# Kernel optimization log

Measured on AMD Instinct MI355X. Metric: run time of the kernel, lower is better.

Reference implementation:

```python
import jax, jax.numpy as jnp
import numpy as np

B, T_ENC, D_IN, H, C, STEPS = 512, 64, 512, 512, 38, 26


def setup_inputs() -> dict:
    key = jax.random.key(0)
    ks = jax.random.split(key, 12)
    s = 0.05
    return {
        "encoder_output": jax.random.normal(ks[0], (B, T_ENC, D_IN), jnp.float32),
        "text": jax.random.randint(ks[1], (B, STEPS), 0, C),
        "w_i2h": jax.random.normal(ks[2], (H, D_IN), jnp.float32) * s,
        "w_h2h": jax.random.normal(ks[3], (H, H), jnp.float32) * s,
        "b_h2h": jax.random.normal(ks[4], (H,), jnp.float32) * s,
        "w_score": jax.random.normal(ks[5], (1, H), jnp.float32) * s,
        "w_ih": jax.random.normal(ks[6], (4 * H, D_IN + C), jnp.float32) * s,
        "w_hh": jax.random.normal(ks[7], (4 * H, H), jnp.float32) * s,
        "b_ih": jax.random.normal(ks[8], (4 * H,), jnp.float32) * s,
        "b_hh": jax.random.normal(ks[9], (4 * H,), jnp.float32) * s,
        "w_gen": jax.random.normal(ks[10], (C, H), jnp.float32) * s,
        "b_gen": jax.random.normal(ks[11], (C,), jnp.float32) * s,
    }


def reference(encoder_output, text, w_i2h, w_h2h, b_h2h, w_score, w_ih, w_hh,
              b_ih, b_hh, w_gen, b_gen):
    # i2h(batch_H) is step-invariant -> hoist out of the decode loop (same math).
    H_proj = jnp.einsum('btd,hd->bth', encoder_output, w_i2h)  # [B,T,H]
    onehots = jax.nn.one_hot(text, C, dtype=encoder_output.dtype)  # [B,S,C]
    oh_seq = jnp.swapaxes(onehots, 0, 1)  # [S,B,C]

    def step(carry, oh):
        h, c = carry
        hp = (h @ w_h2h.T + b_h2h)[:, None, :]                 # [B,1,H]
        e = jnp.tanh(H_proj + hp) @ w_score[0]                  # [B,T]
        alpha = jax.nn.softmax(e, axis=1)                       # [B,T]
        context = jnp.einsum('bt,btd->bd', alpha, encoder_output)
        x = jnp.concatenate([context, oh], axis=1)              # [B,D+C]
        gates = x @ w_ih.T + b_ih + h @ w_hh.T + b_hh           # [B,4H]
        i_g, f_g, g_g, o_g = jnp.split(gates, 4, axis=1)
        c_new = jax.nn.sigmoid(f_g) * c + jax.nn.sigmoid(i_g) * jnp.tanh(g_g)
        h_new = jax.nn.sigmoid(o_g) * jnp.tanh(c_new)
        return (h_new, c_new), h_new

    z = jnp.zeros((encoder_output.shape[0], w_h2h.shape[0]), encoder_output.dtype)
    _, hs = jax.lax.scan(step, (z, z), oh_seq)                  # hs: [S,B,H]
    hiddens = jnp.swapaxes(hs, 0, 1)                            # [B,S,H]
    probs = hiddens @ w_gen.T + b_gen                           # [B,S,C]
    return probs
```

## Files before the change

### kernel.cpp

```cpp
#include <hip/hip_runtime.h>

typedef __attribute__((ext_vector_type(8))) short bf16x8;
typedef __attribute__((ext_vector_type(4))) float f32x4;
typedef __attribute__((ext_vector_type(4))) int   i32x4;

#define DEV static __device__ __forceinline__

constexpr int BATCH = 512;
constexpr int TENC  = 64;
constexpr int DIN   = 512;
constexpr int HDIM  = 512;
constexpr int NCLS  = 38;
constexpr int STEPS = 26;
constexpr int NG    = 4 * HDIM;

constexpr size_t HP_OFF   = 0;
constexpr size_t HP_SZ    = (size_t)BATCH * TENC * HDIM * 2;
constexpr size_t ENC_OFF  = HP_OFF + HP_SZ;
constexpr size_t ENC_SZ   = (size_t)BATCH * TENC * DIN * 2;
constexpr size_t A2_OFF   = ENC_OFF + ENC_SZ;
constexpr size_t A2_SZ    = (size_t)2 * BATCH * 1024 * 2;
constexpr size_t HP32_OFF = A2_OFF + A2_SZ;
constexpr size_t HP32_SZ  = (size_t)BATCH * HDIM * 4;
constexpr size_t B2R_OFF  = HP32_OFF + HP32_SZ;
constexpr size_t B2R_SZ   = (size_t)NG * 1024 * 2;
constexpr size_t WI2H_OFF = B2R_OFF + B2R_SZ;
constexpr size_t WI2H_SZ  = (size_t)HDIM * DIN * 2;
constexpr size_t B3_OFF   = WI2H_OFF + WI2H_SZ;
constexpr size_t B3_SZ    = (size_t)576 * HDIM * 2;
constexpr size_t WOH_OFF  = B3_OFF + B3_SZ;
constexpr size_t WOH_SZ   = (size_t)NG * NCLS * 4;
constexpr size_t BIAS_OFF = WOH_OFF + WOH_SZ;
constexpr size_t BIAS_SZ  = (size_t)NG * 4;
constexpr size_t HSEQ_OFF = BIAS_OFF + BIAS_SZ;
constexpr size_t HSEQ_SZ  = (size_t)STEPS * BATCH * HDIM * 2;
constexpr size_t BAR_OFF  = HSEQ_OFF + HSEQ_SZ;
constexpr size_t BAR_SZ   = 32768;

DEV float bf2f(unsigned short s) {
    unsigned u = ((unsigned)s) << 16;
    return __builtin_bit_cast(float, u);
}
DEV unsigned short f2bf(float f) {
    unsigned u = __builtin_bit_cast(unsigned, f);
    u = (u + 0x7fffu + ((u >> 16) & 1u)) >> 16;
    return (unsigned short)u;
}
DEV float sigmoid_f(float x) { return 1.f / (1.f + __expf(-x)); }
DEV float tanh_f(float x) {
    x = fminf(fmaxf(x, -15.f), 15.f);
    float e = __expf(2.f * x);
    return (e - 1.f) / (e + 1.f);
}

DEV unsigned aload(const unsigned* p) {
    return __hip_atomic_load(p, __ATOMIC_RELAXED, __HIP_MEMORY_SCOPE_AGENT);
}
DEV unsigned long long aload64(const unsigned long long* p) {
    return __hip_atomic_load(p, __ATOMIC_RELAXED, __HIP_MEMORY_SCOPE_AGENT);
}
DEV float aloadf(const float* p) {
    return __hip_atomic_load(p, __ATOMIC_RELAXED, __HIP_MEMORY_SCOPE_AGENT);
}
DEV void astore(unsigned* p, unsigned v) {
    __hip_atomic_store(p, v, __ATOMIC_RELAXED, __HIP_MEMORY_SCOPE_AGENT);
}
DEV void astoref(float* p, float v) {
    __hip_atomic_store(p, v, __ATOMIC_RELAXED, __HIP_MEMORY_SCOPE_AGENT);
}
DEV bf16x8 mk_frag(unsigned long long lo, unsigned long long hi) {
    union { unsigned long long q[2]; bf16x8 v; } u;
    u.q[0] = lo; u.q[1] = hi;
    return u.v;
}

DEV void gbar(unsigned* gb, int j, unsigned g) {
    __syncthreads();
    if (threadIdx.x == 0) {
        const int sg = j & 3;
        unsigned* sub  = gb + sg * 32;
        unsigned* root = gb + 128;
        unsigned* genp = gb + 160 + sg * 32;
        bool flipped = false;
        if (__hip_atomic_fetch_add(sub, 1u, __ATOMIC_RELAXED, __HIP_MEMORY_SCOPE_AGENT) == g * 8u - 1u) {
            if (__hip_atomic_fetch_add(root, 1u, __ATOMIC_RELAXED, __HIP_MEMORY_SCOPE_AGENT) == g * 4u - 1u) {
                #pragma unroll
                for (int i = 0; i < 4; i++) astore(gb + 160 + i * 32, g);
                flipped = true;
            }
        }
        if (!flipped) {
            while (aload(genp) < g) __builtin_amdgcn_s_sleep(1);
        }
    }
    __syncthreads();
}

__global__ void conv_bf16_kernel(const float* __restrict__ in,
                                 unsigned short* __restrict__ out, int n4) {
    int i = blockIdx.x * blockDim.x + threadIdx.x;
    int stride = gridDim.x * blockDim.x;
    for (; i < n4; i += stride) {
        float4 v = ((const float4*)in)[i];
        ushort4 o;
        o.x = f2bf(v.x); o.y = f2bf(v.y); o.z = f2bf(v.z); o.w = f2bf(v.w);
        ((ushort4*)out)[i] = o;
    }
}

__global__ void build_b2r_kernel(const float* __restrict__ w_ih, const float* __restrict__ w_hh,
                                 const float* __restrict__ b_ih, const float* __restrict__ b_hh,
                                 unsigned short* __restrict__ B2r, float* __restrict__ woh,
                                 float* __restrict__ bias2r) {
    int np = blockIdx.x;
    int u = np >> 2, g = np & 3;
    int src = g * 512 + u;
    for (int k = threadIdx.x; k < 512; k += blockDim.x) {
        B2r[np * 1024 + k]       = f2bf(w_ih[src * 550 + k]);
        B2r[np * 1024 + 512 + k] = f2bf(w_hh[src * 512 + k]);
    }
    if (threadIdx.x < NCLS) woh[np * NCLS + threadIdx.x] = w_ih[src * 550 + 512 + threadIdx.x];
    if (threadIdx.x == 0)   bias2r[np] = b_ih[src] + b_hh[src];
}

__global__ void build_b3_kernel(const float* __restrict__ w_h2h, const float* __restrict__ w_gen,
                                unsigned short* __restrict__ B3) {
    int n = blockIdx.x;
    for (int k = threadIdx.x; k < 512; k += blockDim.x) {
        float v = 0.f;
        if (n < 512)      v = w_h2h[n * 512 + k];
        else if (n < 550) v = w_gen[(n - 512) * 512 + k];
        B3[n * 512 + k] = f2bf(v);
    }
}

__global__ void init_state_kernel(unsigned short* __restrict__ A2,
                                  unsigned* __restrict__ bar) {
    int b = blockIdx.x;
    for (int j = threadIdx.x; j < 512; j += blockDim.x)
        A2[b * 1024 + 512 + j] = 0;
    if (b == 0)
        for (int j = threadIdx.x; j < 8192; j += blockDim.x) bar[j] = 0;
}

template<int BM, int BN, int WN, int FRM, int FRN>
DEV void gemm_core(const unsigned short* __restrict__ A, int ldA,
                   const unsigned short* __restrict__ Bm, int ldB, int K,
                   int m0, int n0, unsigned short* __restrict__ lA,
                   unsigned short* __restrict__ lB, f32x4 acc[FRM][FRN]) {
    constexpr int LSTR = 40;
    const int tid  = threadIdx.x;
    const int lane = tid & 63;
    const int wid  = tid >> 6;
    const int wm = wid / WN, wn = wid % WN;
    const int fr_row = lane & 15;
    const int fr_kb  = (lane >> 4) * 8;

    for (int k0 = 0; k0 < K; k0 += 32) {
        for (int u = tid; u < BM * 4; u += 256) {
            int r = u >> 2, cb = u & 3;
            *(i32x4*)(lA + r * LSTR + cb * 8) =
                *(const i32x4*)(A + (size_t)(m0 + r) * ldA + k0 + cb * 8);
        }
        for (int u = tid; u < BN * 4; u += 256) {
            int r = u >> 2, cb = u & 3;
            *(i32x4*)(lB + r * LSTR + cb * 8) =
                *(const i32x4*)(Bm + (size_t)(n0 + r) * ldB + k0 + cb * 8);
        }
        __syncthreads();
        bf16x8 af[FRM], bfv[FRN];
        #pragma unroll
        for (int i = 0; i < FRM; i++)
            af[i] = *(const bf16x8*)(lA + (wm * FRM * 16 + i * 16 + fr_row) * LSTR + fr_kb);
        #pragma unroll
        for (int j = 0; j < FRN; j++)
            bfv[j] = *(const bf16x8*)(lB + (wn * FRN * 16 + j * 16 + fr_row) * LSTR + fr_kb);
        #pragma unroll
        for (int i = 0; i < FRM; i++)
            #pragma unroll
            for (int j = 0; j < FRN; j++)
                acc[i][j] = __builtin_amdgcn_mfma_f32_16x16x32_bf16(af[i], bfv[j], acc[i][j], 0, 0, 0);
        __syncthreads();
    }
}

__global__ __launch_bounds__(256) void gemm_bf16out_kernel(
    const unsigned short* __restrict__ A, int ldA,
    const unsigned short* __restrict__ Bm, int ldB,
    unsigned short* __restrict__ C, int ldC, int K) {
    constexpr int BM = 128, BN = 128, FRM = 4, FRN = 4;
    __shared__ __align__(16) unsigned short lA[BM * 40], lB[BN * 40];
    int m0 = blockIdx.x * BM, n0 = blockIdx.y * BN;
    f32x4 acc[FRM][FRN] = {};
    gemm_core<BM, BN, 2, FRM, FRN>(A, ldA, Bm, ldB, K, m0, n0, lA, lB, acc);
    const int lane = threadIdx.x & 63, wid = threadIdx.x >> 6;
    const int wm = wid >> 1, wn = wid & 1;
    #pragma unroll
    for (int i = 0; i < FRM; i++)
        #pragma unroll
        for (int j = 0; j < FRN; j++)
            #pragma unroll
            for (int r = 0; r < 4; r++) {
                int m = m0 + wm * FRM * 16 + i * 16 + (lane >> 4) * 4 + r;
                int n = n0 + wn * FRN * 16 + j * 16 + (lane & 15);
                C[(size_t)m * ldC + n] = f2bf(acc[i][j][r]);
            }
}

__global__ __launch_bounds__(256) void probs_kernel(
    const unsigned short* __restrict__ hseq,
    const unsigned short* __restrict__ Bg,
    const float* __restrict__ b_gen, float* __restrict__ out) {
    __shared__ __align__(16) unsigned short lA[64 * 40], lB[64 * 40];
    int m0 = blockIdx.x * 64;
    f32x4 acc[2][2] = {};
    gemm_core<64, 64, 2, 2, 2>(hseq, 512, Bg, 512, 512, m0, 0, lA, lB, acc);
    const int lane = threadIdx.x & 63, wid = threadIdx.x >> 6;
    const int wm = wid >> 1, wn = wid & 1;
    #pragma unroll
    for (int i = 0; i < 2; i++)
        #pragma unroll
        for (int j = 0; j < 2; j++)
            #pragma unroll
            for (int r = 0; r < 4; r++) {
                int m = m0 + wm * 32 + i * 16 + (lane >> 4) * 4 + r;
                int n = wn * 32 + j * 16 + (lane & 15);
                if (n < NCLS) {
                    int ss = m >> 9, b = m & 511;
                    out[((size_t)b * STEPS + ss) * NCLS + n] = acc[i][j][r] + b_gen[n];
                }
            }
}

__global__ __launch_bounds__(512, 2) void decode_kernel(
    const unsigned short* __restrict__ Hp,
    const unsigned short* __restrict__ enc,
    unsigned short* __restrict__ A2,
    float* __restrict__ hpb,
    const unsigned short* __restrict__ B2r,
    const float* __restrict__ bias2r,
    const float* __restrict__ woh,
    const unsigned short* __restrict__ B3,
    const float* __restrict__ b_h2h,
    const float* __restrict__ w_score,
    const int* __restrict__ text,
    unsigned short* __restrict__ hseq,
    unsigned* __restrict__ bar) {
    __shared__ __align__(16) unsigned short lB2w[64 * 1032];
    __shared__ __align__(16) char scr[17408];

    const int bid  = blockIdx.x;
    const int tid  = threadIdx.x;
    const int lane = tid & 63, wid = tid >> 6;
    const int grp = bid >> 5;
    const int j   = bid & 31;
    const int gm0 = grp * 64;
    const int ng0 = j * 64;
    const int ncol0 = j * 16;
    const int mi = wid & 3;
    const int kh = wid >> 2;
    unsigned* gb = bar + grp * 1024;

    for (int u = tid; u < 8192; u += 512) {
        int r = u >> 7, cb = u & 127;
        *(i32x4*)(lB2w + r * 1032 + cb * 8) =
            *(const i32x4*)(B2r + (size_t)(ng0 + r) * 1024 + cb * 8);
    }

    float c0 = 0.f, c1 = 0.f;
    unsigned gen = 0;

    float* pbuf  = (float*)scr;
    float* e_lds = (float*)scr;
    float* al_lds = e_lds + 128;
    float* gbuf  = (float*)scr;

    for (int s = 0; s < STEPS; ++s) {
        unsigned short* A2cur = A2 + (size_t)(s & 1) * BATCH * 1024;
        unsigned short* A2nxt = A2 + (size_t)((s + 1) & 1) * BATCH * 1024;

        {
            const int arow = gm0 + mi * 16 + (lane & 15);
            const unsigned long long* Ah = (const unsigned long long*)
                (A2cur + (size_t)arow * 1024 + 512 + kh * 256 + (lane >> 4) * 8);
            const unsigned short* wrow = B3 + (size_t)(ncol0 + (lane & 15)) * 512
                                            + kh * 256 + (lane >> 4) * 8;
            unsigned long long h0v[8], h1v[8];
            #pragma unroll
            for (int kc = 0; kc < 8; ++kc) {
                h0v[kc] = aload64(Ah + kc * 8);
                h1v[kc] = aload64(Ah + kc * 8 + 1);
            }
            f32x4 acc = {};
            #pragma unroll
            for (int kc = 0; kc < 8; ++kc) {
                bf16x8 af = mk_frag(h0v[kc], h1v[kc]);
                bf16x8 bf = *(const bf16x8*)(wrow + kc * 32);
                acc = __builtin_amdgcn_mfma_f32_16x16x32_bf16(af, bf, acc, 0, 0, 0);
            }
            if (kh == 1) {
                #pragma unroll
                for (int r = 0; r < 4; r++)
                    pbuf[mi * 272 + ((lane >> 4) * 4 + r) * 17 + (lane & 15)] = acc[r];
            }
            __syncthreads();
            if (kh == 0) {
                #pragma unroll
                for (int r = 0; r < 4; r++) {
                    int row = (lane >> 4) * 4 + r, col = lane & 15;
                    float v = acc[r] + pbuf[mi * 272 + row * 17 + col] + b_h2h[ncol0 + col];
                    astoref(hpb + (size_t)(gm0 + mi * 16 + row) * 512 + ncol0 + col, v);
                }
            }
        }
        gbar(gb, j, ++gen);

        f32x4 gacc[4] = {};
        {
            unsigned long long g0v[16], g1v[16];
            if (kh == 1) {
                const unsigned long long* Ag = (const unsigned long long*)
                    (A2cur + (size_t)(gm0 + mi * 16 + (lane & 15)) * 1024 + 512 + (lane >> 4) * 8);
                #pragma unroll
                for (int kc = 0; kc < 16; ++kc) {
                    g0v[kc] = aload64(Ag + kc * 8);
                    g1v[kc] = aload64(Ag + kc * 8 + 1);
                }
            }

            const int half = tid >> 8, t4 = tid & 255, w4 = t4 >> 6;
            const int b = gm0 + 2 * j + half;
            float hp8[8], ws8[8];
            #pragma unroll
            for (int q = 0; q < 8; q++) hp8[q] = aloadf(hpb + (size_t)b * 512 + lane * 8 + q);
            {
                const float4* wsp = (const float4*)(w_score + lane * 8);
                float4 w0 = wsp[0], w1 = wsp[1];
                ws8[0] = w0.x; ws8[1] = w0.y; ws8[2] = w0.z; ws8[3] = w0.w;
                ws8[4] = w1.x; ws8[5] = w1.y; ws8[6] = w1.z; ws8[7] = w1.w;
            }
            for (int t = w4; t < 64; t += 4) {
                bf16x8 hv = *(const bf16x8*)(Hp + ((size_t)b * 64 + t) * 512 + lane * 8);
                float a = 0.f;
                #pragma unroll
                for (int q = 0; q < 8; q++)
                    a += ws8[q] * tanh_f(hp8[q] + bf2f((unsigned short)hv[q]));
                #pragma unroll
                for (int off = 32; off > 0; off >>= 1) a += __shfl_down(a, off);
                if (lane == 0) e_lds[half * 64 + t] = a;
            }
            __syncthreads();
            if (w4 == 0) {
                float v = e_lds[half * 64 + lane];
                float m = v;
                #pragma unroll
                for (int off = 32; off > 0; off >>= 1) m = fmaxf(m, __shfl_xor(m, off));
                float ex = __expf(v - m);
                float sum = ex;
                #pragma unroll
                for (int off = 32; off > 0; off >>= 1) sum += __shfl_xor(sum, off);
                al_lds[half * 64 + lane] = ex / sum;
            }
            __syncthreads();
            float a0 = 0.f, a1 = 0.f;
            const unsigned short* erow = enc + (size_t)b * 64 * 512 + t4 * 2;
            #pragma unroll 8
            for (int t = 0; t < 64; t++) {
                float al = al_lds[half * 64 + t];
                unsigned pv = *(const unsigned*)(erow + (size_t)t * 512);
                a0 += al * bf2f((unsigned short)(pv & 0xffffu));
                a1 += al * bf2f((unsigned short)(pv >> 16));
            }
            unsigned pk = ((unsigned)f2bf(a1) << 16) | (unsigned)f2bf(a0);
            astore((unsigned*)(A2cur + (size_t)b * 1024) + t4, pk);

            if (kh == 1) {
                #pragma unroll
                for (int kc = 0; kc < 16; ++kc) {
                    bf16x8 af = mk_frag(g0v[kc], g1v[kc]);
                    #pragma unroll
                    for (int nj = 0; nj < 4; ++nj) {
                        bf16x8 bf = *(const bf16x8*)(lB2w + (nj * 16 + (lane & 15)) * 1032
                                                     + 512 + (lane >> 4) * 8 + kc * 32);
                        gacc[nj] = __builtin_amdgcn_mfma_f32_16x16x32_bf16(af, bf, gacc[nj], 0, 0, 0);
                    }
                }
            }
        }
        gbar(gb, j, ++gen);

        {
            if (kh == 0) {
                const unsigned long long* Ac = (const unsigned long long*)
                    (A2cur + (size_t)(gm0 + mi * 16 + (lane & 15)) * 1024 + (lane >> 4) * 8);
                unsigned long long c0v[16], c1v[16];
                #pragma unroll
                for (int kc = 0; kc < 16; ++kc) {
                    c0v[kc] = aload64(Ac + kc * 8);
                    c1v[kc] = aload64(Ac + kc * 8 + 1);
                }
                #pragma unroll
                for (int kc = 0; kc < 16; ++kc) {
                    bf16x8 af = mk_frag(c0v[kc], c1v[kc]);
                    #pragma unroll
                    for (int nj = 0; nj < 4; ++nj) {
                        bf16x8 bf = *(const bf16x8*)(lB2w + (nj * 16 + (lane & 15)) * 1032
                                                     + (lane >> 4) * 8 + kc * 32);
                        gacc[nj] = __builtin_amdgcn_mfma_f32_16x16x32_bf16(af, bf, gacc[nj], 0, 0, 0);
                    }
                }
            }
            const int grow = mi * 16 + (lane >> 4) * 4;
            const int gcol = lane & 15;
            if (kh == 1) {
                #pragma unroll
                for (int nj = 0; nj < 4; ++nj)
                    #pragma unroll
                    for (int r = 0; r < 4; r++)
                        gbuf[(grow + r) * 68 + nj * 16 + gcol] = gacc[nj][r];
            }
            __syncthreads();
            if (kh == 0) {
                #pragma unroll
                for (int nj = 0; nj < 4; ++nj)
                    #pragma unroll
                    for (int r = 0; r < 4; r++)
                        gbuf[(grow + r) * 68 + nj * 16 + gcol] += gacc[nj][r];
            }
            __syncthreads();
            {
                const int rl = tid >> 3, q = tid & 7;
                const int b = gm0 + rl;
                const int npb = ng0 + q * 8;
                const int u0 = npb >> 2;
                const int tb = text[b * STEPS + s];
                const float* gr = gbuf + rl * 68 + q * 8;
                float4 g0 = *(const float4*)gr;
                float4 g1 = *(const float4*)(gr + 4);
                float vi0 = g0.x + bias2r[npb + 0] + woh[(npb + 0) * NCLS + tb];
                float vf0 = g0.y + bias2r[npb + 1] + woh[(npb + 1) * NCLS + tb];
                float vg0 = g0.z + bias2r[npb + 2] + woh[(npb + 2) * NCLS + tb];
                float vo0 = g0.w + bias2r[npb + 3] + woh[(npb + 3) * NCLS + tb];
                float vi1 = g1.x + bias2r[npb + 4] + woh[(npb + 4) * NCLS + tb];
                float vf1 = g1.y + bias2r[npb + 5] + woh[(npb + 5) * NCLS + tb];
                float vg1 = g1.z + bias2r[npb + 6] + woh[(npb + 6) * NCLS + tb];
                float vo1 = g1.w + bias2r[npb + 7] + woh[(npb + 7) * NCLS + tb];
                float cn0 = sigmoid_f(vf0) * c0 + sigmoid_f(vi0) * tanh_f(vg0);
                float cn1 = sigmoid_f(vf1) * c1 + sigmoid_f(vi1) * tanh_f(vg1);
                c0 = cn0; c1 = cn1;
                float hn0 = sigmoid_f(vo0) * tanh_f(cn0);
                float hn1 = sigmoid_f(vo1) * tanh_f(cn1);
                unsigned hp2 = ((unsigned)f2bf(hn1) << 16) | (unsigned)f2bf(hn0);
                astore((unsigned*)(A2nxt + (size_t)b * 1024 + 512 + u0), hp2);
                *(unsigned*)(hseq + ((size_t)s * BATCH + b) * 512 + u0) = hp2;
            }
        }
        if (s + 1 < STEPS) gbar(gb, j, ++gen);
    }
}

extern "C" void kernel_launch(void* const* d_in, const int* in_sizes, int n_in,
                              void* d_out, int out_size, void* d_ws, size_t ws_size,
                              hipStream_t stream) {
    (void)in_sizes; (void)n_in; (void)out_size; (void)ws_size;
    const float* enc_f   = (const float*)d_in[0];
    const int*   text    = (const int*)d_in[1];
    const float* w_i2h   = (const float*)d_in[2];
    const float* w_h2h   = (const float*)d_in[3];
    const float* b_h2h   = (const float*)d_in[4];
    const float* w_score = (const float*)d_in[5];
    const float* w_ih    = (const float*)d_in[6];
    const float* w_hh    = (const float*)d_in[7];
    const float* b_ih    = (const float*)d_in[8];
    const float* b_hh    = (const float*)d_in[9];
    const float* w_gen   = (const float*)d_in[10];
    const float* b_gen   = (const float*)d_in[11];
    float* out = (float*)d_out;

    char* ws = (char*)d_ws;
    const unsigned short* Hp     = (const unsigned short*)(ws + HP_OFF);
    unsigned short*       Hp_w   = (unsigned short*)(ws + HP_OFF);
    const unsigned short* encb   = (const unsigned short*)(ws + ENC_OFF);
    unsigned short*       encb_w = (unsigned short*)(ws + ENC_OFF);
    unsigned short*       A2     = (unsigned short*)(ws + A2_OFF);
    float*                hpb    = (float*)(ws + HP32_OFF);
    const unsigned short* B2r    = (const unsigned short*)(ws + B2R_OFF);
    unsigned short*       B2r_w  = (unsigned short*)(ws + B2R_OFF);
    unsigned short*       wi2hb  = (unsigned short*)(ws + WI2H_OFF);
    const unsigned short* B3     = (const unsigned short*)(ws + B3_OFF);
    unsigned short*       B3_w   = (unsigned short*)(ws + B3_OFF);
    const float*          woh    = (const float*)(ws + WOH_OFF);
    float*                woh_w  = (float*)(ws + WOH_OFF);
    const float*          bias2r = (const float*)(ws + BIAS_OFF);
    float*                bias2r_w = (float*)(ws + BIAS_OFF);
    unsigned short*       hseq   = (unsigned short*)(ws + HSEQ_OFF);
    unsigned*             bar    = (unsigned*)(ws + BAR_OFF);

    conv_bf16_kernel<<<2048, 256, 0, stream>>>(enc_f, encb_w, BATCH * TENC * DIN / 4);
    conv_bf16_kernel<<<256, 256, 0, stream>>>(w_i2h, wi2hb, HDIM * DIN / 4);
    build_b2r_kernel<<<NG, 256, 0, stream>>>(w_ih, w_hh, b_ih, b_hh, B2r_w, woh_w, bias2r_w);
    build_b3_kernel<<<576, 256, 0, stream>>>(w_h2h, w_gen, B3_w);
    init_state_kernel<<<BATCH, 256, 0, stream>>>(A2, bar);

    gemm_bf16out_kernel<<<dim3(BATCH * TENC / 128, HDIM / 128), 256, 0, stream>>>(
        encb, DIN, wi2hb, DIN, Hp_w, HDIM, DIN);

    {
        void* args[13] = {
            (void*)&Hp, (void*)&encb, (void*)&A2, (void*)&hpb,
            (void*)&B2r, (void*)&bias2r, (void*)&woh, (void*)&B3,
            (void*)&b_h2h, (void*)&w_score, (void*)&text, (void*)&hseq, (void*)&bar
        };
        hipLaunchCooperativeKernel((const void*)decode_kernel, dim3(256), dim3(512),
                                   args, 0, stream);
    }

    probs_kernel<<<dim3(STEPS * BATCH / 64), 256, 0, stream>>>(
        hseq, B3 + (size_t)512 * 512, b_gen, out);
}
```

Measured before the change: 1.134 ms.

## Compute h2h projection redundantly per block to drop one grid barrier per step

Each block now loads only the two hidden rows it needs for attention into LDS and computes their full 512-wide h2h projection locally via MFMA, writing into shared memory. Previously the projection was partitioned across the 32 blocks of a group, written to a global fp32 buffer, and required a group barrier before attention could read it. That barrier and the global buffer are removed, and the h-part gate MFMA is moved ahead of the attention phase. The cost is redundant work: every block reads the full 512x512 w_h2h from global or L2 each step, and MFMA tiles run with only 2 of 16 rows used. Launch bounds also drop the min-2-blocks hint.

Result: slower. 1.832 ms (+61.5%).

```diff
diff --git a/kernel.cpp b/kernel.cpp
--- a/kernel.cpp
+++ b/kernel.cpp
@@ -20,9 +20,7 @@
 constexpr size_t ENC_SZ   = (size_t)BATCH * TENC * DIN * 2;
 constexpr size_t A2_OFF   = ENC_OFF + ENC_SZ;
 constexpr size_t A2_SZ    = (size_t)2 * BATCH * 1024 * 2;
-constexpr size_t HP32_OFF = A2_OFF + A2_SZ;
-constexpr size_t HP32_SZ  = (size_t)BATCH * HDIM * 4;
-constexpr size_t B2R_OFF  = HP32_OFF + HP32_SZ;
+constexpr size_t B2R_OFF  = A2_OFF + A2_SZ;
 constexpr size_t B2R_SZ   = (size_t)NG * 1024 * 2;
 constexpr size_t WI2H_OFF = B2R_OFF + B2R_SZ;
 constexpr size_t WI2H_SZ  = (size_t)HDIM * DIN * 2;
@@ -59,13 +57,7 @@
 DEV unsigned long long aload64(const unsigned long long* p) {
     return __hip_atomic_load(p, __ATOMIC_RELAXED, __HIP_MEMORY_SCOPE_AGENT);
 }
-DEV float aloadf(const float* p) {
-    return __hip_atomic_load(p, __ATOMIC_RELAXED, __HIP_MEMORY_SCOPE_AGENT);
-}
 DEV void astore(unsigned* p, unsigned v) {
-    __hip_atomic_store(p, v, __ATOMIC_RELAXED, __HIP_MEMORY_SCOPE_AGENT);
-}
-DEV void astoref(float* p, float v) {
     __hip_atomic_store(p, v, __ATOMIC_RELAXED, __HIP_MEMORY_SCOPE_AGENT);
 }
 DEV bf16x8 mk_frag(unsigned long long lo, unsigned long long hi) {
@@ -232,11 +224,10 @@
             }
 }
 
-__global__ __launch_bounds__(512, 2) void decode_kernel(
+__global__ __launch_bounds__(512) void decode_kernel(
     const unsigned short* __restrict__ Hp,
     const unsigned short* __restrict__ enc,
     unsigned short* __restrict__ A2,
-    float* __restrict__ hpb,
     const unsigned short* __restrict__ B2r,
     const float* __restrict__ bias2r,
     const float* __restrict__ woh,
@@ -248,6 +239,8 @@
     unsigned* __restrict__ bar) {
     __shared__ __align__(16) unsigned short lB2w[64 * 1032];
     __shared__ __align__(16) char scr[17408];
+    __shared__ __align__(16) unsigned short hl[2 * 520];
+    __shared__ __align__(16) float hp_l[2 * 512];
 
     const int bid  = blockIdx.x;
     const int tid  = threadIdx.x;
@@ -256,7 +249,6 @@
     const int j   = bid & 31;
     const int gm0 = grp * 64;
     const int ng0 = j * 64;
-    const int ncol0 = j * 16;
     const int mi = wid & 3;
     const int kh = wid >> 2;
     unsigned* gb = bar + grp * 1024;
@@ -270,69 +262,79 @@
     float c0 = 0.f, c1 = 0.f;
     unsigned gen = 0;
 
-    float* pbuf  = (float*)scr;
-    float* e_lds = (float*)scr;
+    float* e_lds  = (float*)scr;
     float* al_lds = e_lds + 128;
-    float* gbuf  = (float*)scr;
+    float* gbuf   = (float*)scr;
 
     for (int s = 0; s < STEPS; ++s) {
         unsigned short* A2cur = A2 + (size_t)(s & 1) * BATCH * 1024;
         unsigned short* A2nxt = A2 + (size_t)((s + 1) & 1) * BATCH * 1024;
 
         {
-            const int arow = gm0 + mi * 16 + (lane & 15);
-            const unsigned long long* Ah = (const unsigned long long*)
-                (A2cur + (size_t)arow * 1024 + 512 + kh * 256 + (lane >> 4) * 8);
-            const unsigned short* wrow = B3 + (size_t)(ncol0 + (lane & 15)) * 512
-                                            + kh * 256 + (lane >> 4) * 8;
-            unsigned long long h0v[8], h1v[8];
-            #pragma unroll
-            for (int kc = 0; kc < 8; ++kc) {
-                h0v[kc] = aload64(Ah + kc * 8);
-                h1v[kc] = aload64(Ah + kc * 8 + 1);
-            }
-            f32x4 acc = {};
-            #pragma unroll
-            for (int kc = 0; kc < 8; ++kc) {
-                bf16x8 af = mk_frag(h0v[kc], h1v[kc]);
-                bf16x8 bf = *(const bf16x8*)(wrow + kc * 32);
-                acc = __builtin_amdgcn_mfma_f32_16x16x32_bf16(af, bf, acc, 0, 0, 0);
-            }
-            if (kh == 1) {
-                #pragma unroll
-                for (int r = 0; r < 4; r++)
-                    pbuf[mi * 272 + ((lane >> 4) * 4 + r) * 17 + (lane & 15)] = acc[r];
-            }
-            __syncthreads();
-            if (kh == 0) {
-                #pragma unroll
-                for (int r = 0; r < 4; r++) {
-                    int row = (lane >> 4) * 4 + r, col = lane & 15;
-                    float v = acc[r] + pbuf[mi * 272 + row * 17 + col] + b_h2h[ncol0 + col];
-                    astoref(hpb + (size_t)(gm0 + mi * 16 + row) * 512 + ncol0 + col, v);
+            const int r = tid >> 8, jc = tid & 255;
+            unsigned hv = aload((const unsigned*)(A2cur + (size_t)(gm0 + 2 * j + r) * 1024 + 512) + jc);
+            *(unsigned*)(hl + r * 520 + jc * 2) = hv;
+        }
+
+        unsigned long long g0v[16], g1v[16];
+        if (kh == 1) {
+            const unsigned long long* Ag = (const unsigned long long*)
+                (A2cur + (size_t)(gm0 + mi * 16 + (lane & 15)) * 1024 + 512 + (lane >> 4) * 8);
+            #pragma unroll
+            for (int kc = 0; kc < 16; ++kc) {
+                g0v[kc] = aload64(Ag + kc * 8);
+                g1v[kc] = aload64(Ag + kc * 8 + 1);
+            }
+        }
+        __syncthreads();
+
+        {
+            const int prow = lane & 15;
+            const unsigned short* hlr = hl + (prow < 2 ? prow : 0) * 520 + (lane >> 4) * 8;
+            f32x4 pacc[4] = {};
+            #pragma unroll
+            for (int kc = 0; kc < 16; ++kc) {
+                bf16x8 af = *(const bf16x8*)(hlr + kc * 32);
+                #pragma unroll
+                for (int ct = 0; ct < 4; ++ct) {
+                    const unsigned short* wrow = B3 + (size_t)(wid * 64 + ct * 16 + prow) * 512
+                                                    + kc * 32 + (lane >> 4) * 8;
+                    bf16x8 bf = *(const bf16x8*)wrow;
+                    pacc[ct] = __builtin_amdgcn_mfma_f32_16x16x32_bf16(af, bf, pacc[ct], 0, 0, 0);
                 }
             }
-        }
-        gbar(gb, j, ++gen);
+            if ((lane >> 4) == 0) {
+                #pragma unroll
+                for (int ct = 0; ct < 4; ++ct) {
+                    int col = wid * 64 + ct * 16 + (lane & 15);
+                    float bh = b_h2h[col];
+                    hp_l[col]       = pacc[ct][0] + bh;
+                    hp_l[512 + col] = pacc[ct][1] + bh;
+                }
+            }
+        }
 
         f32x4 gacc[4] = {};
+        if (kh == 1) {
+            #pragma unroll
+            for (int kc = 0; kc < 16; ++kc) {
+                bf16x8 af = mk_frag(g0v[kc], g1v[kc]);
+                #pragma unroll
+                for (int nj = 0; nj < 4; ++nj) {
+                    bf16x8 bf = *(const bf16x8*)(lB2w + (nj * 16 + (lane & 15)) * 1032
+                                                 + 512 + (lane >> 4) * 8 + kc * 32);
+                    gacc[nj] = __builtin_amdgcn_mfma_f32_16x16x32_bf16(af, bf, gacc[nj], 0, 0, 0);
+                }
+            }
+        }
+        __syncthreads();
+
         {
-            unsigned long long g0v[16], g1v[16];
-            if (kh == 1) {
-                const unsigned long long* Ag = (const unsigned long long*)
-                    (A2cur + (size_t)(gm0 + mi * 16 + (lane & 15)) * 1024 + 512 + (lane >> 4) * 8);
-                #pragma unroll
-                for (int kc = 0; kc < 16; ++kc) {
-                    g0v[kc] = aload64(Ag + kc * 8);
-                    g1v[kc] = aload64(Ag + kc * 8 + 1);
-                }
-            }
-
             const int half = tid >> 8, t4 = tid & 255, w4 = t4 >> 6;
             const int b = gm0 + 2 * j + half;
             float hp8[8], ws8[8];
             #pragma unroll
-            for (int q = 0; q < 8; q++) hp8[q] = aloadf(hpb + (size_t)b * 512 + lane * 8 + q);
+            for (int q = 0; q < 8; q++) hp8[q] = hp_l[half * 512 + lane * 8 + q];
             {
                 const float4* wsp = (const float4*)(w_score + lane * 8);
                 float4 w0 = wsp[0], w1 = wsp[1];
@@ -373,19 +375,6 @@
             }
             unsigned pk = ((unsigned)f2bf(a1) << 16) | (unsigned)f2bf(a0);
             astore((unsigned*)(A2cur + (size_t)b * 1024) + t4, pk);
-
-            if (kh == 1) {
-                #pragma unroll
-                for (int kc = 0; kc < 16; ++kc) {
-                    bf16x8 af = mk_frag(g0v[kc], g1v[kc]);
-                    #pragma unroll
-                    for (int nj = 0; nj < 4; ++nj) {
-                        bf16x8 bf = *(const bf16x8*)(lB2w + (nj * 16 + (lane & 15)) * 1032
-                                                     + 512 + (lane >> 4) * 8 + kc * 32);
-                        gacc[nj] = __builtin_amdgcn_mfma_f32_16x16x32_bf16(af, bf, gacc[nj], 0, 0, 0);
-                    }
-                }
-            }
         }
         gbar(gb, j, ++gen);
 
@@ -483,7 +472,6 @@
     const unsigned short* encb   = (const unsigned short*)(ws + ENC_OFF);
     unsigned short*       encb_w = (unsigned short*)(ws + ENC_OFF);
     unsigned short*       A2     = (unsigned short*)(ws + A2_OFF);
-    float*                hpb    = (float*)(ws + HP32_OFF);
     const unsigned short* B2r    = (const unsigned short*)(ws + B2R_OFF);
     unsigned short*       B2r_w  = (unsigned short*)(ws + B2R_OFF);
     unsigned short*       wi2hb  = (unsigned short*)(ws + WI2H_OFF);
@@ -506,8 +494,8 @@
         encb, DIN, wi2hb, DIN, Hp_w, HDIM, DIN);
 
     {
-        void* args[13] = {
-            (void*)&Hp, (void*)&encb, (void*)&A2, (void*)&hpb,
+        void* args[12] = {
+            (void*)&Hp, (void*)&encb, (void*)&A2,
             (void*)&B2r, (void*)&bias2r, (void*)&woh, (void*)&B3,
             (void*)&b_h2h, (void*)&w_score, (void*)&text, (void*)&hseq, (void*)&bar
         };
```

## Split grid barrier into arrive/wait and overlap h-part gate MFMA with barrier

Applied to the files above, without the earlier changes.

Replaces the hierarchical tree barrier with a flat per-group counter, split into separate arrive and wait phases. Between arrive and wait, the kernel prefetches the step's Hp rows into registers and runs the h-part of the gate GEMM using the h fragments already loaded for the h2h projection. This hides barrier latency and removes the redundant h reload. The context-part GEMM is now split across both wave halves by K instead of one half doing all 16 chunks. It also drops the launch_bounds minimum of 2 blocks per CU, which raises register pressure headroom but may change residency and contention on the single counter.

After: 1.228 ms. 8.2% more time.

```diff
diff --git a/kernel.cpp b/kernel.cpp
--- a/kernel.cpp
+++ b/kernel.cpp
@@ -74,24 +74,14 @@
     return u.v;
 }
 
-DEV void gbar(unsigned* gb, int j, unsigned g) {
+DEV void gbar_arrive(unsigned* ctr) {
     __syncthreads();
+    if (threadIdx.x == 0)
+        __hip_atomic_fetch_add(ctr, 1u, __ATOMIC_RELAXED, __HIP_MEMORY_SCOPE_AGENT);
+}
+DEV void gbar_wait(unsigned* ctr, unsigned g) {
     if (threadIdx.x == 0) {
-        const int sg = j & 3;
-        unsigned* sub  = gb + sg * 32;
-        unsigned* root = gb + 128;
-        unsigned* genp = gb + 160 + sg * 32;
-        bool flipped = false;
-        if (__hip_atomic_fetch_add(sub, 1u, __ATOMIC_RELAXED, __HIP_MEMORY_SCOPE_AGENT) == g * 8u - 1u) {
-            if (__hip_atomic_fetch_add(root, 1u, __ATOMIC_RELAXED, __HIP_MEMORY_SCOPE_AGENT) == g * 4u - 1u) {
-                #pragma unroll
-                for (int i = 0; i < 4; i++) astore(gb + 160 + i * 32, g);
-                flipped = true;
-            }
-        }
-        if (!flipped) {
-            while (aload(genp) < g) __builtin_amdgcn_s_sleep(1);
-        }
+        while (aload(ctr) < g * 32u) __builtin_amdgcn_s_sleep(1);
     }
     __syncthreads();
 }
@@ -232,7 +222,7 @@
             }
 }
 
-__global__ __launch_bounds__(512, 2) void decode_kernel(
+__global__ __launch_bounds__(512) void decode_kernel(
     const unsigned short* __restrict__ Hp,
     const unsigned short* __restrict__ enc,
     unsigned short* __restrict__ A2,
@@ -259,7 +249,7 @@
     const int ncol0 = j * 16;
     const int mi = wid & 3;
     const int kh = wid >> 2;
-    unsigned* gb = bar + grp * 1024;
+    unsigned* ctr = bar + grp * 256;
 
     for (int u = tid; u < 8192; u += 512) {
         int r = u >> 7, cb = u & 127;
@@ -275,22 +265,25 @@
     float* al_lds = e_lds + 128;
     float* gbuf  = (float*)scr;
 
+    const int half = tid >> 8, t4 = tid & 255, w4 = t4 >> 6;
+    const int ab = gm0 + 2 * j + half;
+
     for (int s = 0; s < STEPS; ++s) {
         unsigned short* A2cur = A2 + (size_t)(s & 1) * BATCH * 1024;
         unsigned short* A2nxt = A2 + (size_t)((s + 1) & 1) * BATCH * 1024;
 
+        unsigned long long h0v[8], h1v[8];
         {
-            const int arow = gm0 + mi * 16 + (lane & 15);
             const unsigned long long* Ah = (const unsigned long long*)
-                (A2cur + (size_t)arow * 1024 + 512 + kh * 256 + (lane >> 4) * 8);
-            const unsigned short* wrow = B3 + (size_t)(ncol0 + (lane & 15)) * 512
-                                            + kh * 256 + (lane >> 4) * 8;
-            unsigned long long h0v[8], h1v[8];
+                (A2cur + (size_t)(gm0 + mi * 16 + (lane & 15)) * 1024 + 512
+                 + kh * 256 + (lane >> 4) * 8);
             #pragma unroll
             for (int kc = 0; kc < 8; ++kc) {
                 h0v[kc] = aload64(Ah + kc * 8);
                 h1v[kc] = aload64(Ah + kc * 8 + 1);
             }
+            const unsigned short* wrow = B3 + (size_t)(ncol0 + (lane & 15)) * 512
+                                            + kh * 256 + (lane >> 4) * 8;
             f32x4 acc = {};
             #pragma unroll
             for (int kc = 0; kc < 8; ++kc) {
@@ -313,38 +306,44 @@
                 }
             }
         }
-        gbar(gb, j, ++gen);
-
+        gbar_arrive(ctr); ++gen;
+
+        bf16x8 hpv[16];
+        #pragma unroll
+        for (int tt = 0; tt < 16; ++tt) {
+            int t = w4 + tt * 4;
+            hpv[tt] = *(const bf16x8*)(Hp + ((size_t)ab * 64 + t) * 512 + lane * 8);
+        }
         f32x4 gacc[4] = {};
+        #pragma unroll
+        for (int kc = 0; kc < 8; ++kc) {
+            bf16x8 af = mk_frag(h0v[kc], h1v[kc]);
+            #pragma unroll
+            for (int nj = 0; nj < 4; ++nj) {
+                bf16x8 bf = *(const bf16x8*)(lB2w + (nj * 16 + (lane & 15)) * 1032
+                                             + 512 + kh * 256 + (lane >> 4) * 8 + kc * 32);
+                gacc[nj] = __builtin_amdgcn_mfma_f32_16x16x32_bf16(af, bf, gacc[nj], 0, 0, 0);
+            }
+        }
+        gbar_wait(ctr, gen);
+
         {
-            unsigned long long g0v[16], g1v[16];
-            if (kh == 1) {
-                const unsigned long long* Ag = (const unsigned long long*)
-                    (A2cur + (size_t)(gm0 + mi * 16 + (lane & 15)) * 1024 + 512 + (lane >> 4) * 8);
-                #pragma unroll
-                for (int kc = 0; kc < 16; ++kc) {
-                    g0v[kc] = aload64(Ag + kc * 8);
-                    g1v[kc] = aload64(Ag + kc * 8 + 1);
-                }
-            }
-
-            const int half = tid >> 8, t4 = tid & 255, w4 = t4 >> 6;
-            const int b = gm0 + 2 * j + half;
             float hp8[8], ws8[8];
             #pragma unroll
-            for (int q = 0; q < 8; q++) hp8[q] = aloadf(hpb + (size_t)b * 512 + lane * 8 + q);
+            for (int q = 0; q < 8; q++) hp8[q] = aloadf(hpb + (size_t)ab * 512 + lane * 8 + q);
             {
                 const float4* wsp = (const float4*)(w_score + lane * 8);
                 float4 w0 = wsp[0], w1 = wsp[1];
                 ws8[0] = w0.x; ws8[1] = w0.y; ws8[2] = w0.z; ws8[3] = w0.w;
                 ws8[4] = w1.x; ws8[5] = w1.y; ws8[6] = w1.z; ws8[7] = w1.w;
             }
-            for (int t = w4; t < 64; t += 4) {
-                bf16x8 hv = *(const bf16x8*)(Hp + ((size_t)b * 64 + t) * 512 + lane * 8);
+            #pragma unroll
+            for (int tt = 0; tt < 16; ++tt) {
+                int t = w4 + tt * 4;
                 float a = 0.f;
                 #pragma unroll
                 for (int q = 0; q < 8; q++)
-                    a += ws8[q] * tanh_f(hp8[q] + bf2f((unsigned short)hv[q]));
+                    a += ws8[q] * tanh_f(hp8[q] + bf2f((unsigned short)hpv[tt][q]));
                 #pragma unroll
                 for (int off = 32; off > 0; off >>= 1) a += __shfl_down(a, off);
                 if (lane == 0) e_lds[half * 64 + t] = a;
@@ -363,7 +362,7 @@
             }
             __syncthreads();
             float a0 = 0.f, a1 = 0.f;
-            const unsigned short* erow = enc + (size_t)b * 64 * 512 + t4 * 2;
+            const unsigned short* erow = enc + (size_t)ab * 64 * 512 + t4 * 2;
             #pragma unroll 8
             for (int t = 0; t < 64; t++) {
                 float al = al_lds[half * 64 + t];
@@ -372,42 +371,29 @@
                 a1 += al * bf2f((unsigned short)(pv >> 16));
             }
             unsigned pk = ((unsigned)f2bf(a1) << 16) | (unsigned)f2bf(a0);
-            astore((unsigned*)(A2cur + (size_t)b * 1024) + t4, pk);
-
-            if (kh == 1) {
-                #pragma unroll
-                for (int kc = 0; kc < 16; ++kc) {
-                    bf16x8 af = mk_frag(g0v[kc], g1v[kc]);
-                    #pragma unroll
-                    for (int nj = 0; nj < 4; ++nj) {
-                        bf16x8 bf = *(const bf16x8*)(lB2w + (nj * 16 + (lane & 15)) * 1032
-                                                     + 512 + (lane >> 4) * 8 + kc * 32);
-                        gacc[nj] = __builtin_amdgcn_mfma_f32_16x16x32_bf16(af, bf, gacc[nj], 0, 0, 0);
-                    }
-                }
-            }
-        }
-        gbar(gb, j, ++gen);
+            astore((unsigned*)(A2cur + (size_t)ab * 1024) + t4, pk);
+        }
+        gbar_arrive(ctr); ++gen;
+        gbar_wait(ctr, gen);
 
         {
-            if (kh == 0) {
-                const unsigned long long* Ac = (const unsigned long long*)
-                    (A2cur + (size_t)(gm0 + mi * 16 + (lane & 15)) * 1024 + (lane >> 4) * 8);
-                unsigned long long c0v[16], c1v[16];
-                #pragma unroll
-                for (int kc = 0; kc < 16; ++kc) {
-                    c0v[kc] = aload64(Ac + kc * 8);
-                    c1v[kc] = aload64(Ac + kc * 8 + 1);
-                }
-                #pragma unroll
-                for (int kc = 0; kc < 16; ++kc) {
-                    bf16x8 af = mk_frag(c0v[kc], c1v[kc]);
-                    #pragma unroll
-                    for (int nj = 0; nj < 4; ++nj) {
-                        bf16x8 bf = *(const bf16x8*)(lB2w + (nj * 16 + (lane & 15)) * 1032
-                                                     + (lane >> 4) * 8 + kc * 32);
-                        gacc[nj] = __builtin_amdgcn_mfma_f32_16x16x32_bf16(af, bf, gacc[nj], 0, 0, 0);
-                    }
+            const unsigned long long* Ac = (const unsigned long long*)
+                (A2cur + (size_t)(gm0 + mi * 16 + (lane & 15)) * 1024
+                 + kh * 256 + (lane >> 4) * 8);
+            unsigned long long c0v[8], c1v[8];
+            #pragma unroll
+            for (int kc = 0; kc < 8; ++kc) {
+                c0v[kc] = aload64(Ac + kc * 8);
+                c1v[kc] = aload64(Ac + kc * 8 + 1);
+            }
+            #pragma unroll
+            for (int kc = 0; kc < 8; ++kc) {
+                bf16x8 af = mk_frag(c0v[kc], c1v[kc]);
+                #pragma unroll
+                for (int nj = 0; nj < 4; ++nj) {
+                    bf16x8 bf = *(const bf16x8*)(lB2w + (nj * 16 + (lane & 15)) * 1032
+                                                 + kh * 256 + (lane >> 4) * 8 + kc * 32);
+                    gacc[nj] = __builtin_amdgcn_mfma_f32_16x16x32_bf16(af, bf, gacc[nj], 0, 0, 0);
                 }
             }
             const int grow = mi * 16 + (lane >> 4) * 4;
@@ -455,7 +441,10 @@
                 *(unsigned*)(hseq + ((size_t)s * BATCH + b) * 512 + u0) = hp2;
             }
         }
-        if (s + 1 < STEPS) gbar(gb, j, ++gen);
+        if (s + 1 < STEPS) {
+            gbar_arrive(ctr); ++gen;
+            gbar_wait(ctr, gen);
+        }
     }
 }
 
```
